# Kernel tuning notes

Hardware: AMD Instinct MI355X
Metric: run time of the kernel (lower is better)

Reference implementation:

```python
import jax, jax.numpy as jnp
import numpy as np

B, N, L, D = 4, 2048, 12, 128  # batch, nodes, in_len, d_model


def _glorot(key, shape):
    fan_in = shape[0]
    return jax.random.normal(key, shape, dtype=jnp.float32) / jnp.sqrt(jnp.float32(fan_in))


def setup_inputs() -> dict:
    key = jax.random.key(0)
    ks = jax.random.split(key, 12)
    x = jax.random.normal(ks[0], (B, N, L, D), dtype=jnp.float32)
    adj = jax.random.uniform(ks[1], (N, N), dtype=jnp.float32)  # dense weighted adjacency
    # mlp2: Linear(L*D -> D)
    W_mlp2 = _glorot(ks[2], (L * D, D)); b_mlp2 = jnp.zeros((D,), jnp.float32)
    # GNN: three DenseSAGEConv layers (lin_rel on aggregated, lin_root on self)
    Wr1 = _glorot(ks[3], (D, D)); Wo1 = _glorot(ks[4], (D, D)); b1 = jnp.zeros((D,), jnp.float32)
    Wr2 = _glorot(ks[5], (D, D)); Wo2 = _glorot(ks[6], (D, D)); b2 = jnp.zeros((D,), jnp.float32)
    Wr3 = _glorot(ks[7], (D, D)); Wo3 = _glorot(ks[8], (D, D)); b3 = jnp.zeros((D,), jnp.float32)
    # mlp1: Linear(D -> L*D)
    W_mlp1 = _glorot(ks[9], (D, L * D)); b_mlp1 = jnp.zeros((L * D,), jnp.float32)
    return {"x": x, "adj": adj, "W_mlp2": W_mlp2, "b_mlp2": b_mlp2,
            "Wr1": Wr1, "Wo1": Wo1, "b1": b1,
            "Wr2": Wr2, "Wo2": Wo2, "b2": b2,
            "Wr3": Wr3, "Wo3": Wo3, "b3": b3,
            "W_mlp1": W_mlp1, "b_mlp1": b_mlp1}


def reference(x, adj, W_mlp2, b_mlp2, Wr1, Wo1, b1, Wr2, Wo2, b2, Wr3, Wo3, b3, W_mlp1, b_mlp1):
    b_, n_, l_, d_ = x.shape
    xf = x.reshape(b_, n_, l_ * d_)                      # 'b n l d -> b n (l d)'
    h = xf @ W_mlp2 + b_mlp2                             # mlp2: (B,N,D)
    deg = jnp.clip(adj.sum(axis=-1, keepdims=True), 1.0, None)  # (N,1)

    def sage(hin, Wr, Wo, bb):
        # mean neighbor aggregation: (adj @ h) / deg, then rel + root linear
        agg = jnp.einsum('mn,bnd->bmd', adj, hin) / deg
        return agg @ Wr + hin @ Wo + bb

    h = jax.nn.relu(sage(h, Wr1, Wo1, b1))
    h = jax.nn.relu(sage(h, Wr2, Wo2, b2))
    h = sage(h, Wr3, Wo3, b3)                            # gnn1_embed output (B,N,D)
    out = h @ W_mlp1 + b_mlp1                            # mlp1: (B,N,L*D)
    return out
```

## Files before the change

### kernel.cpp

```cpp
#include <hip/hip_runtime.h>

typedef __attribute__((ext_vector_type(8))) short short8;
typedef __attribute__((ext_vector_type(4))) short short4v;
typedef __attribute__((ext_vector_type(4))) float floatx4;

__device__ inline short to_bf16s(float f) {
    unsigned u = __builtin_bit_cast(unsigned, f);
    unsigned r = u + 0x7FFFu + ((u >> 16) & 1u);
    return (short)(r >> 16);
}

__device__ inline void dma16(const short* g, short* l) {
    __builtin_amdgcn_global_load_lds(
        (const __attribute__((address_space(1))) unsigned int*)(const void*)g,
        (__attribute__((address_space(3))) unsigned int*)(void*)l,
        16, 0, 0);
}

template <typename T> struct Ld8;
template <> struct Ld8<short> {
    static __device__ inline short8 load(const short* p) { return *(const short8*)p; }
};
template <> struct Ld8<float> {
    static __device__ inline short8 load(const float* p) {
        float4 f0 = *(const float4*)p;
        float4 f1 = *(const float4*)(p + 4);
        short8 r;
        r[0] = to_bf16s(f0.x); r[1] = to_bf16s(f0.y);
        r[2] = to_bf16s(f0.z); r[3] = to_bf16s(f0.w);
        r[4] = to_bf16s(f1.x); r[5] = to_bf16s(f1.y);
        r[6] = to_bf16s(f1.z); r[7] = to_bf16s(f1.w);
        return r;
    }
};

struct PrepArgs {
    const float* adj;
    const float* W2; const float* W1;
    const float* Wr0; const float* Wo0;
    const float* Wr1; const float* Wo1;
    const float* Wr2; const float* Wo2;
    short* adjS; short* W2T; short* W1T;
    short* BigB0; short* BigB1; short* BigB2;
};

__global__ __launch_bounds__(256) void prep(PrepArgs p) {
    int bid = blockIdx.x;
    if (bid < 2048) {
        const float* src = p.adj + (size_t)bid * 2048;
        float s = 0.f;
        for (int c = threadIdx.x; c < 2048; c += 256) s += src[c];
        __shared__ float red[256];
        red[threadIdx.x] = s;
        __syncthreads();
        for (int st = 128; st > 0; st >>= 1) {
            if (threadIdx.x < st) red[threadIdx.x] += red[threadIdx.x + st];
            __syncthreads();
        }
        float d = red[0];
        d = d < 1.f ? 1.f : d;
        float inv = 1.f / d;
        short* dst = p.adjS + (size_t)bid * 2048;
        for (int c = threadIdx.x; c < 2048; c += 256) dst[c] = to_bf16s(src[c] * inv);
        return;
    }
    int t = bid - 2048;
    __shared__ short tile[32][33];
    int tx = threadIdx.x & 31, ty0 = threadIdx.x >> 5;
    const float* in; int C_; int bx, by;
    short* outp; int outld, copies, copystride, outofs;
    if (t < 192) {
        bx = (t & 3) * 32; by = (t >> 2) * 32; in = p.W2; C_ = 128;
        outp = p.W2T; outld = 1536; copies = 1; copystride = 0; outofs = 0;
    } else if (t < 384) {
        int u = t - 192; bx = (u % 48) * 32; by = (u / 48) * 32; in = p.W1; C_ = 1536;
        outp = p.W1T; outld = 128; copies = 1; copystride = 0; outofs = 0;
    } else {
        int u = t - 384; int l = u / 32; int v = u % 32;
        const float* Wr[3] = {p.Wr0, p.Wr1, p.Wr2};
        const float* Wo[3] = {p.Wo0, p.Wo1, p.Wo2};
        short* BB[3] = {p.BigB0, p.BigB1, p.BigB2};
        outp = BB[l]; outld = 640; C_ = 128;
        if (v < 16) { in = Wr[l]; bx = (v & 3) * 32; by = (v >> 2) * 32;
                      copies = 4; copystride = 128; outofs = 0; }
        else { v -= 16; in = Wo[l]; bx = (v & 3) * 32; by = (v >> 2) * 32;
               copies = 1; copystride = 0; outofs = 512; }
    }
    for (int i = ty0; i < 32; i += 8)
        tile[i][tx] = to_bf16s(in[(size_t)(by + i) * C_ + bx + tx]);
    __syncthreads();
    for (int i = ty0; i < 32; i += 8) {
        short v = tile[tx][i];
        for (int c = 0; c < copies; ++c)
            outp[(size_t)(bx + i) * outld + (by + tx) + outofs + c * copystride] = v;
    }
}

#define LDSTR 72

template <typename TA, int RELU, int ROWMAP, int HTW>
__global__ __launch_bounds__(256) void gemmT(
    const TA* __restrict__ A, int lda,
    const short* __restrict__ B, int ldb, int kTiles,
    const float* __restrict__ bias,
    short* __restrict__ C, int ldc, int colofs,
    short* __restrict__ HT) {
    __shared__ __align__(16) short lds[2 * 96 * LDSTR];

    int tid = threadIdx.x;
    int blockM = blockIdx.x * 32;
    int blockN = blockIdx.y * 64;

    int srow = tid >> 3;
    int scol = (tid & 7) * 8;

    const TA* Abase = A + (size_t)blockM * lda;
    const short* Bbase = B + (size_t)blockN * ldb;

    short8 ra, rb0, rb1;
    ra  = Ld8<TA>::load(Abase + (size_t)srow * lda + scol);
    rb0 = Ld8<short>::load(Bbase + (size_t)srow * ldb + scol);
    rb1 = Ld8<short>::load(Bbase + (size_t)(srow + 32) * ldb + scol);

    floatx4 acc[2];
    #pragma unroll
    for (int j = 0; j < 2; ++j)
        #pragma unroll
        for (int r = 0; r < 4; ++r) acc[j][r] = 0.f;

    int lane = tid & 63;
    int w = tid >> 6;
    int wr = w >> 1, wc = w & 1;
    int quad = lane >> 4, l15 = lane & 15;

    for (int it = 0; it < kTiles; ++it) {
        short* As = lds + (it & 1) * (96 * LDSTR);
        short* Bs = As + 32 * LDSTR;
        *(short8*)(As + srow * LDSTR + scol) = ra;
        *(short8*)(Bs + srow * LDSTR + scol) = rb0;
        *(short8*)(Bs + (srow + 32) * LDSTR + scol) = rb1;
        __syncthreads();
        if (it + 1 < kTiles) {
            int ko = (it + 1) * 64;
            ra  = Ld8<TA>::load(Abase + (size_t)srow * lda + ko + scol);
            rb0 = Ld8<short>::load(Bbase + (size_t)srow * ldb + ko + scol);
            rb1 = Ld8<short>::load(Bbase + (size_t)(srow + 32) * ldb + ko + scol);
        }
        const short* Arow = As + (wr * 16 + l15) * LDSTR;
        const short* Brow = Bs + (wc * 32 + l15) * LDSTR;
        #pragma unroll
        for (int ks = 0; ks < 2; ++ks) {
            int kof = ks * 32 + quad * 8;
            short8 a0 = *(const short8*)(Arow + kof);
            short8 b0 = *(const short8*)(Brow + kof);
            short8 b1 = *(const short8*)(Brow + 16 * LDSTR + kof);
            acc[0] = __builtin_amdgcn_mfma_f32_16x16x32_bf16(a0, b0, acc[0], 0, 0, 0);
            acc[1] = __builtin_amdgcn_mfma_f32_16x16x32_bf16(a0, b1, acc[1], 0, 0, 0);
        }
        __syncthreads();
    }

    #pragma unroll
    for (int tj = 0; tj < 2; ++tj) {
        int col = blockN + wc * 32 + tj * 16 + l15;
        float bv = bias[col];
        int m0 = blockM + wr * 16 + quad * 4;
        short4v pk;
        #pragma unroll
        for (int r = 0; r < 4; ++r) {
            int m = m0 + r;
            float xv = acc[tj][r] + bv;
            if (RELU) xv = xv > 0.f ? xv : 0.f;
            short v = to_bf16s(xv);
            pk[r] = v;
            int orow = ROWMAP ? (((m & 2047) << 2) | (m >> 11)) : m;
            C[(size_t)orow * ldc + col + colofs] = v;
            if (HTW && !ROWMAP) {
                HT[(size_t)((m & 3) * 128 + col) * 2048 + (m >> 2)] = v;
            }
        }
        if (HTW && ROWMAP) {
            int b = m0 >> 11, n0 = m0 & 2047;
            *(short4v*)(HT + (size_t)(b * 128 + col) * 2048 + n0) = pk;
        }
    }
}

__global__ __launch_bounds__(256) void gemmS(const short* __restrict__ A,
                                             const short* __restrict__ B,
                                             short* __restrict__ C) {
    __shared__ __align__(16) short As[64 * 64];
    __shared__ __align__(16) short Bs[128 * 64];

    int tid = threadIdx.x;
    int blockM = blockIdx.x * 64;
    int blockN = blockIdx.y * 128;
    int kz = blockIdx.z * 512;

    const short* Ab = A + (size_t)(blockM + (tid >> 3)) * 2048 + kz + (tid & 7) * 8;
    const short* Bb = B + (size_t)(blockN + (tid >> 3)) * 2048 + kz + (tid & 7) * 8;
    short* Al = As + tid * 8;
    short* Bl = Bs + tid * 8;

    floatx4 acc[2][4];
    #pragma unroll
    for (int i = 0; i < 2; ++i)
        #pragma unroll
        for (int j = 0; j < 4; ++j)
            #pragma unroll
            for (int r = 0; r < 4; ++r) acc[i][j][r] = 0.f;

    int lane = tid & 63;
    int w = tid >> 6;
    int wr = w >> 1, wc = w & 1;
    int quad = lane >> 4, l15 = lane & 15;

    for (int it = 0; it < 8; ++it) {
        const short* Ag = Ab + it * 64;
        const short* Bg = Bb + it * 64;
        dma16(Ag, Al);
        dma16(Ag + (size_t)32 * 2048, Al + 2048);
        #pragma unroll
        for (int r = 0; r < 4; ++r)
            dma16(Bg + (size_t)r * 32 * 2048, Bl + r * 2048);
        __syncthreads();
        const short* Ar = As + (wr * 32 + l15) * 64;
        const short* Br = Bs + (wc * 64 + l15) * 64;
        #pragma unroll
        for (int ks = 0; ks < 2; ++ks) {
            int kof = ks * 32 + quad * 8;
            short8 af[2], bfr[4];
            #pragma unroll
            for (int i = 0; i < 2; ++i) af[i] = *(const short8*)(Ar + i * 16 * 64 + kof);
            #pragma unroll
            for (int j = 0; j < 4; ++j) bfr[j] = *(const short8*)(Br + j * 16 * 64 + kof);
            #pragma unroll
            for (int i = 0; i < 2; ++i)
                #pragma unroll
                for (int j = 0; j < 4; ++j)
                    acc[i][j] = __builtin_amdgcn_mfma_f32_16x16x32_bf16(af[i], bfr[j], acc[i][j], 0, 0, 0);
        }
        __syncthreads();
    }

    int colofs = blockIdx.z * 128;
    #pragma unroll
    for (int ti = 0; ti < 2; ++ti) {
        #pragma unroll
        for (int tj = 0; tj < 4; ++tj) {
            int j = blockN + wc * 64 + tj * 16 + l15;
            int jhi = j >> 7, jlo = j & 127;
            int row0 = blockM + wr * 32 + ti * 16 + quad * 4;
            #pragma unroll
            for (int r = 0; r < 4; ++r) {
                int m = row0 + r;
                C[(size_t)(m * 4 + jhi) * 640 + jlo + colofs] = to_bf16s(acc[ti][tj][r]);
            }
        }
    }
}

template <int MODE>
__global__ __launch_bounds__(256) void gemm128(
    const short* __restrict__ A, int lda,
    const short* __restrict__ B, int ldb,
    int kChunkIters, const float* __restrict__ bias,
    void* __restrict__ Cv, int ldc) {
    __shared__ __align__(16) short As[128 * 64];
    __shared__ __align__(16) short Bs[128 * 64];

    int tid = threadIdx.x;
    int blockM = blockIdx.x * 128;
    int blockN = blockIdx.y * 128;
    int kz = blockIdx.z * kChunkIters * 64;

    const short* Ab = A + (size_t)(blockM + (tid >> 3)) * lda + kz + (tid & 7) * 8;
    const short* Bb = B + (size_t)(blockN + (tid >> 3)) * ldb + kz + (tid & 7) * 8;
    short* Al = As + tid * 8;
    short* Bl = Bs + tid * 8;

    floatx4 acc[4][4];
    #pragma unroll
    for (int i = 0; i < 4; ++i)
        #pragma unroll
        for (int j = 0; j < 4; ++j)
            #pragma unroll
            for (int r = 0; r < 4; ++r) acc[i][j][r] = 0.f;

    int lane = tid & 63;
    int w = tid >> 6;
    int wr = w >> 1, wc = w & 1;
    int quad = lane >> 4, l15 = lane & 15;

    for (int it = 0; it < kChunkIters; ++it) {
        const short* Ag = Ab + it * 64;
        const short* Bg = Bb + it * 64;
        #pragma unroll
        for (int r = 0; r < 4; ++r) {
            dma16(Ag + (size_t)r * 32 * lda, Al + r * 2048);
            dma16(Bg + (size_t)r * 32 * ldb, Bl + r * 2048);
        }
        __syncthreads();
        const short* Ar = As + (wr * 64 + l15) * 64;
        const short* Br = Bs + (wc * 64 + l15) * 64;
        #pragma unroll
        for (int ks = 0; ks < 2; ++ks) {
            int kof = ks * 32 + quad * 8;
            short8 af[4], bfr[4];
            #pragma unroll
            for (int i = 0; i < 4; ++i) af[i] = *(const short8*)(Ar + i * 16 * 64 + kof);
            #pragma unroll
            for (int j = 0; j < 4; ++j) bfr[j] = *(const short8*)(Br + j * 16 * 64 + kof);
            #pragma unroll
            for (int i = 0; i < 4; ++i)
                #pragma unroll
                for (int j = 0; j < 4; ++j)
                    acc[i][j] = __builtin_amdgcn_mfma_f32_16x16x32_bf16(af[i], bfr[j], acc[i][j], 0, 0, 0);
        }
        __syncthreads();
    }

    {
        float* Cf = (float*)Cv;
        #pragma unroll
        for (int ti = 0; ti < 4; ++ti) {
            #pragma unroll
            for (int tj = 0; tj < 4; ++tj) {
                int col = blockN + wc * 64 + tj * 16 + l15;
                float bv = bias[col];
                int row0 = blockM + wr * 64 + ti * 16 + quad * 4;
                #pragma unroll
                for (int r = 0; r < 4; ++r) {
                    int mp = row0 + r;
                    int orow = ((mp & 3) << 11) | (mp >> 2);
                    Cf[(size_t)orow * ldc + col] = acc[ti][tj][r] + bv;
                }
            }
        }
    }
}

extern "C" void kernel_launch(void* const* d_in, const int* in_sizes, int n_in,
                              void* d_out, int out_size, void* d_ws, size_t ws_size,
                              hipStream_t stream) {
    const float* x      = (const float*)d_in[0];
    const float* adj    = (const float*)d_in[1];
    const float* W_mlp2 = (const float*)d_in[2];
    const float* b_mlp2 = (const float*)d_in[3];
    const float* Wr1    = (const float*)d_in[4];
    const float* Wo1    = (const float*)d_in[5];
    const float* b1     = (const float*)d_in[6];
    const float* Wr2    = (const float*)d_in[7];
    const float* Wo2    = (const float*)d_in[8];
    const float* b2     = (const float*)d_in[9];
    const float* Wr3    = (const float*)d_in[10];
    const float* Wo3    = (const float*)d_in[11];
    const float* b3     = (const float*)d_in[12];
    const float* W_mlp1 = (const float*)d_in[13];
    const float* b_mlp1 = (const float*)d_in[14];
    float* out = (float*)d_out;

    char* ws = (char*)d_ws;
    size_t off = 0;
    auto alloc = [&](size_t bytes) -> char* {
        char* p = ws + off;
        off = (off + bytes + 255) & ~(size_t)255;
        return p;
    };
    short* W2T  = (short*)alloc(128 * 1536 * 2);
    short* W1T  = (short*)alloc(1536 * 128 * 2);
    short* BigB[3];
    for (int l = 0; l < 3; ++l) BigB[l] = (short*)alloc(128 * 640 * 2);
    short* adjS = (short*)alloc((size_t)2048 * 2048 * 2);
    short* big[4];
    for (int l = 0; l < 4; ++l) big[l] = (short*)alloc((size_t)8192 * 640 * 2);
    short* HT = (short*)alloc((size_t)512 * 2048 * 2);

    dim3 blk(256);

    PrepArgs pa{adj, W_mlp2, W_mlp1, Wr1, Wo1, Wr2, Wo2, Wr3, Wo3,
                adjS, W2T, W1T, BigB[0], BigB[1], BigB[2]};
    prep<<<2528, blk, 0, stream>>>(pa);

    gemmT<float, 0, 1, 1><<<dim3(256, 2), blk, 0, stream>>>(
        x, 1536, W2T, 1536, 24, b_mlp2, big[0], 640, 512, HT);

    for (int l = 0; l < 3; ++l) {
        gemmS<<<dim3(32, 4, 4), blk, 0, stream>>>(adjS, HT, big[l]);
        if (l == 0)
            gemmT<short, 1, 0, 1><<<dim3(256, 2), blk, 0, stream>>>(
                big[0], 640, BigB[0], 640, 10, b1, big[1], 640, 512, HT);
        else if (l == 1)
            gemmT<short, 1, 0, 1><<<dim3(256, 2), blk, 0, stream>>>(
                big[1], 640, BigB[1], 640, 10, b2, big[2], 640, 512, HT);
        else
            gemmT<short, 0, 0, 0><<<dim3(256, 2), blk, 0, stream>>>(
                big[2], 640, BigB[2], 640, 10, b3, big[3], 640, 512, nullptr);
    }

    gemm128<2><<<dim3(64, 12, 1), blk, 0, stream>>>(
        big[3] + 512, 640, W1T, 128, 2, b_mlp1, out, 1536);
}
```

Before: 225.6 us.

## Load MFMA fragments directly from global memory, dropping LDS staging in all GEMMs

The three GEMM kernels (gemmT, gemmS, and the final gemm128, now gemmL) no longer stage tiles through shared memory with barriers and direct-to-LDS DMA. Each lane now loads its bf16 fragments straight from global memory in fully unrolled K loops with compile-time trip counts. This removes LDS traffic and __syncthreads stalls, and relies on L1/L2 caching to supply the data reuse that the shared tiles used to provide. The risk is more redundant global or cache traffic, uncoalesced 16-byte per-lane accesses, and higher register pressure from the full unrolling.

```diff
diff --git a/kernel.cpp b/kernel.cpp
--- a/kernel.cpp
+++ b/kernel.cpp
@@ -8,13 +8,6 @@
     unsigned u = __builtin_bit_cast(unsigned, f);
     unsigned r = u + 0x7FFFu + ((u >> 16) & 1u);
     return (short)(r >> 16);
-}
-
-__device__ inline void dma16(const short* g, short* l) {
-    __builtin_amdgcn_global_load_lds(
-        (const __attribute__((address_space(1))) unsigned int*)(const void*)g,
-        (__attribute__((address_space(3))) unsigned int*)(void*)l,
-        16, 0, 0);
 }
 
 template <typename T> struct Ld8;
@@ -96,68 +89,40 @@
     }
 }
 
-#define LDSTR 72
-
-template <typename TA, int RELU, int ROWMAP, int HTW>
+template <typename TA, int KS, int RELU, int ROWMAP, int HTW>
 __global__ __launch_bounds__(256) void gemmT(
     const TA* __restrict__ A, int lda,
-    const short* __restrict__ B, int ldb, int kTiles,
+    const short* __restrict__ B, int ldb,
     const float* __restrict__ bias,
     short* __restrict__ C, int ldc, int colofs,
     short* __restrict__ HT) {
-    __shared__ __align__(16) short lds[2 * 96 * LDSTR];
-
     int tid = threadIdx.x;
-    int blockM = blockIdx.x * 32;
-    int blockN = blockIdx.y * 64;
-
-    int srow = tid >> 3;
-    int scol = (tid & 7) * 8;
-
-    const TA* Abase = A + (size_t)blockM * lda;
-    const short* Bbase = B + (size_t)blockN * ldb;
-
-    short8 ra, rb0, rb1;
-    ra  = Ld8<TA>::load(Abase + (size_t)srow * lda + scol);
-    rb0 = Ld8<short>::load(Bbase + (size_t)srow * ldb + scol);
-    rb1 = Ld8<short>::load(Bbase + (size_t)(srow + 32) * ldb + scol);
-
-    floatx4 acc[2];
-    #pragma unroll
-    for (int j = 0; j < 2; ++j)
-        #pragma unroll
-        for (int r = 0; r < 4; ++r) acc[j][r] = 0.f;
-
     int lane = tid & 63;
     int w = tid >> 6;
     int wr = w >> 1, wc = w & 1;
     int quad = lane >> 4, l15 = lane & 15;
 
-    for (int it = 0; it < kTiles; ++it) {
-        short* As = lds + (it & 1) * (96 * LDSTR);
-        short* Bs = As + 32 * LDSTR;
-        *(short8*)(As + srow * LDSTR + scol) = ra;
-        *(short8*)(Bs + srow * LDSTR + scol) = rb0;
-        *(short8*)(Bs + (srow + 32) * LDSTR + scol) = rb1;
-        __syncthreads();
-        if (it + 1 < kTiles) {
-            int ko = (it + 1) * 64;
-            ra  = Ld8<TA>::load(Abase + (size_t)srow * lda + ko + scol);
-            rb0 = Ld8<short>::load(Bbase + (size_t)srow * ldb + ko + scol);
-            rb1 = Ld8<short>::load(Bbase + (size_t)(srow + 32) * ldb + ko + scol);
-        }
-        const short* Arow = As + (wr * 16 + l15) * LDSTR;
-        const short* Brow = Bs + (wc * 32 + l15) * LDSTR;
-        #pragma unroll
-        for (int ks = 0; ks < 2; ++ks) {
-            int kof = ks * 32 + quad * 8;
-            short8 a0 = *(const short8*)(Arow + kof);
-            short8 b0 = *(const short8*)(Brow + kof);
-            short8 b1 = *(const short8*)(Brow + 16 * LDSTR + kof);
-            acc[0] = __builtin_amdgcn_mfma_f32_16x16x32_bf16(a0, b0, acc[0], 0, 0, 0);
-            acc[1] = __builtin_amdgcn_mfma_f32_16x16x32_bf16(a0, b1, acc[1], 0, 0, 0);
-        }
-        __syncthreads();
+    int blockM = blockIdx.x * 32;
+    int blockN = blockIdx.y * 64;
+
+    const TA* Ap = A + (size_t)(blockM + wr * 16 + l15) * lda + quad * 8;
+    const short* Bp0 = B + (size_t)(blockN + wc * 32 + l15) * ldb + quad * 8;
+    const short* Bp1 = Bp0 + (size_t)16 * ldb;
+
+    floatx4 acc[2];
+    #pragma unroll
+    for (int j = 0; j < 2; ++j)
+        #pragma unroll
+        for (int r = 0; r < 4; ++r) acc[j][r] = 0.f;
+
+    #pragma unroll
+    for (int t = 0; t < KS; ++t) {
+        int kof = t * 32;
+        short8 a0 = Ld8<TA>::load(Ap + kof);
+        short8 b0 = *(const short8*)(Bp0 + kof);
+        short8 b1 = *(const short8*)(Bp1 + kof);
+        acc[0] = __builtin_amdgcn_mfma_f32_16x16x32_bf16(a0, b0, acc[0], 0, 0, 0);
+        acc[1] = __builtin_amdgcn_mfma_f32_16x16x32_bf16(a0, b1, acc[1], 0, 0, 0);
     }
 
     #pragma unroll
@@ -189,58 +154,45 @@
 __global__ __launch_bounds__(256) void gemmS(const short* __restrict__ A,
                                              const short* __restrict__ B,
                                              short* __restrict__ C) {
-    __shared__ __align__(16) short As[64 * 64];
-    __shared__ __align__(16) short Bs[128 * 64];
-
     int tid = threadIdx.x;
-    int blockM = blockIdx.x * 64;
-    int blockN = blockIdx.y * 128;
-    int kz = blockIdx.z * 512;
-
-    const short* Ab = A + (size_t)(blockM + (tid >> 3)) * 2048 + kz + (tid & 7) * 8;
-    const short* Bb = B + (size_t)(blockN + (tid >> 3)) * 2048 + kz + (tid & 7) * 8;
-    short* Al = As + tid * 8;
-    short* Bl = Bs + tid * 8;
-
-    floatx4 acc[2][4];
-    #pragma unroll
-    for (int i = 0; i < 2; ++i)
-        #pragma unroll
-        for (int j = 0; j < 4; ++j)
-            #pragma unroll
-            for (int r = 0; r < 4; ++r) acc[i][j][r] = 0.f;
-
     int lane = tid & 63;
     int w = tid >> 6;
     int wr = w >> 1, wc = w & 1;
     int quad = lane >> 4, l15 = lane & 15;
-
-    for (int it = 0; it < 8; ++it) {
-        const short* Ag = Ab + it * 64;
-        const short* Bg = Bb + it * 64;
-        dma16(Ag, Al);
-        dma16(Ag + (size_t)32 * 2048, Al + 2048);
-        #pragma unroll
-        for (int r = 0; r < 4; ++r)
-            dma16(Bg + (size_t)r * 32 * 2048, Bl + r * 2048);
-        __syncthreads();
-        const short* Ar = As + (wr * 32 + l15) * 64;
-        const short* Br = Bs + (wc * 64 + l15) * 64;
-        #pragma unroll
-        for (int ks = 0; ks < 2; ++ks) {
-            int kof = ks * 32 + quad * 8;
-            short8 af[2], bfr[4];
-            #pragma unroll
-            for (int i = 0; i < 2; ++i) af[i] = *(const short8*)(Ar + i * 16 * 64 + kof);
-            #pragma unroll
-            for (int j = 0; j < 4; ++j) bfr[j] = *(const short8*)(Br + j * 16 * 64 + kof);
-            #pragma unroll
-            for (int i = 0; i < 2; ++i)
-                #pragma unroll
-                for (int j = 0; j < 4; ++j)
-                    acc[i][j] = __builtin_amdgcn_mfma_f32_16x16x32_bf16(af[i], bfr[j], acc[i][j], 0, 0, 0);
-        }
-        __syncthreads();
+    int kz = blockIdx.z * 512;
+
+    const short* Ap0 = A + (size_t)(blockIdx.x * 64 + wr * 32 + l15) * 2048 + kz + quad * 8;
+    const short* Ap1 = Ap0 + (size_t)16 * 2048;
+    const short* Bp0 = B + (size_t)(blockIdx.y * 128 + wc * 64 + l15) * 2048 + kz + quad * 8;
+    const short* Bp1 = Bp0 + (size_t)16 * 2048;
+    const short* Bp2 = Bp0 + (size_t)32 * 2048;
+    const short* Bp3 = Bp0 + (size_t)48 * 2048;
+
+    floatx4 acc[2][4];
+    #pragma unroll
+    for (int i = 0; i < 2; ++i)
+        #pragma unroll
+        for (int j = 0; j < 4; ++j)
+            #pragma unroll
+            for (int r = 0; r < 4; ++r) acc[i][j][r] = 0.f;
+
+    #pragma unroll
+    for (int t = 0; t < 16; ++t) {
+        int kof = t * 32;
+        short8 a0 = *(const short8*)(Ap0 + kof);
+        short8 a1 = *(const short8*)(Ap1 + kof);
+        short8 b0 = *(const short8*)(Bp0 + kof);
+        short8 b1 = *(const short8*)(Bp1 + kof);
+        short8 b2 = *(const short8*)(Bp2 + kof);
+        short8 b3 = *(const short8*)(Bp3 + kof);
+        acc[0][0] = __builtin_amdgcn_mfma_f32_16x16x32_bf16(a0, b0, acc[0][0], 0, 0, 0);
+        acc[0][1] = __builtin_amdgcn_mfma_f32_16x16x32_bf16(a0, b1, acc[0][1], 0, 0, 0);
+        acc[0][2] = __builtin_amdgcn_mfma_f32_16x16x32_bf16(a0, b2, acc[0][2], 0, 0, 0);
+        acc[0][3] = __builtin_amdgcn_mfma_f32_16x16x32_bf16(a0, b3, acc[0][3], 0, 0, 0);
+        acc[1][0] = __builtin_amdgcn_mfma_f32_16x16x32_bf16(a1, b0, acc[1][0], 0, 0, 0);
+        acc[1][1] = __builtin_amdgcn_mfma_f32_16x16x32_bf16(a1, b1, acc[1][1], 0, 0, 0);
+        acc[1][2] = __builtin_amdgcn_mfma_f32_16x16x32_bf16(a1, b2, acc[1][2], 0, 0, 0);
+        acc[1][3] = __builtin_amdgcn_mfma_f32_16x16x32_bf16(a1, b3, acc[1][3], 0, 0, 0);
     }
 
     int colofs = blockIdx.z * 128;
@@ -248,9 +200,9 @@
     for (int ti = 0; ti < 2; ++ti) {
         #pragma unroll
         for (int tj = 0; tj < 4; ++tj) {
-            int j = blockN + wc * 64 + tj * 16 + l15;
+            int j = blockIdx.y * 128 + wc * 64 + tj * 16 + l15;
             int jhi = j >> 7, jlo = j & 127;
-            int row0 = blockM + wr * 32 + ti * 16 + quad * 4;
+            int row0 = blockIdx.x * 64 + wr * 32 + ti * 16 + quad * 4;
             #pragma unroll
             for (int r = 0; r < 4; ++r) {
                 int m = row0 + r;
@@ -260,81 +212,63 @@
     }
 }
 
-template <int MODE>
-__global__ __launch_bounds__(256) void gemm128(
-    const short* __restrict__ A, int lda,
-    const short* __restrict__ B, int ldb,
-    int kChunkIters, const float* __restrict__ bias,
-    void* __restrict__ Cv, int ldc) {
-    __shared__ __align__(16) short As[128 * 64];
-    __shared__ __align__(16) short Bs[128 * 64];
-
+__global__ __launch_bounds__(256) void gemmL(const short* __restrict__ A,
+                                             const short* __restrict__ B,
+                                             const float* __restrict__ bias,
+                                             float* __restrict__ C) {
     int tid = threadIdx.x;
-    int blockM = blockIdx.x * 128;
-    int blockN = blockIdx.y * 128;
-    int kz = blockIdx.z * kChunkIters * 64;
-
-    const short* Ab = A + (size_t)(blockM + (tid >> 3)) * lda + kz + (tid & 7) * 8;
-    const short* Bb = B + (size_t)(blockN + (tid >> 3)) * ldb + kz + (tid & 7) * 8;
-    short* Al = As + tid * 8;
-    short* Bl = Bs + tid * 8;
-
-    floatx4 acc[4][4];
-    #pragma unroll
-    for (int i = 0; i < 4; ++i)
-        #pragma unroll
-        for (int j = 0; j < 4; ++j)
-            #pragma unroll
-            for (int r = 0; r < 4; ++r) acc[i][j][r] = 0.f;
-
     int lane = tid & 63;
     int w = tid >> 6;
     int wr = w >> 1, wc = w & 1;
     int quad = lane >> 4, l15 = lane & 15;
 
-    for (int it = 0; it < kChunkIters; ++it) {
-        const short* Ag = Ab + it * 64;
-        const short* Bg = Bb + it * 64;
-        #pragma unroll
-        for (int r = 0; r < 4; ++r) {
-            dma16(Ag + (size_t)r * 32 * lda, Al + r * 2048);
-            dma16(Bg + (size_t)r * 32 * ldb, Bl + r * 2048);
-        }
-        __syncthreads();
-        const short* Ar = As + (wr * 64 + l15) * 64;
-        const short* Br = Bs + (wc * 64 + l15) * 64;
-        #pragma unroll
-        for (int ks = 0; ks < 2; ++ks) {
-            int kof = ks * 32 + quad * 8;
-            short8 af[4], bfr[4];
-            #pragma unroll
-            for (int i = 0; i < 4; ++i) af[i] = *(const short8*)(Ar + i * 16 * 64 + kof);
-            #pragma unroll
-            for (int j = 0; j < 4; ++j) bfr[j] = *(const short8*)(Br + j * 16 * 64 + kof);
-            #pragma unroll
-            for (int i = 0; i < 4; ++i)
-                #pragma unroll
-                for (int j = 0; j < 4; ++j)
-                    acc[i][j] = __builtin_amdgcn_mfma_f32_16x16x32_bf16(af[i], bfr[j], acc[i][j], 0, 0, 0);
-        }
-        __syncthreads();
-    }
-
-    {
-        float* Cf = (float*)Cv;
-        #pragma unroll
-        for (int ti = 0; ti < 4; ++ti) {
-            #pragma unroll
-            for (int tj = 0; tj < 4; ++tj) {
-                int col = blockN + wc * 64 + tj * 16 + l15;
-                float bv = bias[col];
-                int row0 = blockM + wr * 64 + ti * 16 + quad * 4;
-                #pragma unroll
-                for (int r = 0; r < 4; ++r) {
-                    int mp = row0 + r;
-                    int orow = ((mp & 3) << 11) | (mp >> 2);
-                    Cf[(size_t)orow * ldc + col] = acc[ti][tj][r] + bv;
-                }
+    int blockM = blockIdx.x * 128;
+    int blockN = blockIdx.y * 128;
+
+    const short* Ap[4];
+    const short* Bp[4];
+    #pragma unroll
+    for (int i = 0; i < 4; ++i)
+        Ap[i] = A + (size_t)(blockM + wr * 64 + i * 16 + l15) * 640 + quad * 8;
+    #pragma unroll
+    for (int j = 0; j < 4; ++j)
+        Bp[j] = B + (size_t)(blockN + wc * 64 + j * 16 + l15) * 128 + quad * 8;
+
+    floatx4 acc[4][4];
+    #pragma unroll
+    for (int i = 0; i < 4; ++i)
+        #pragma unroll
+        for (int j = 0; j < 4; ++j)
+            #pragma unroll
+            for (int r = 0; r < 4; ++r) acc[i][j][r] = 0.f;
+
+    #pragma unroll
+    for (int t = 0; t < 4; ++t) {
+        int kof = t * 32;
+        short8 af[4], bf[4];
+        #pragma unroll
+        for (int i = 0; i < 4; ++i) af[i] = *(const short8*)(Ap[i] + kof);
+        #pragma unroll
+        for (int j = 0; j < 4; ++j) bf[j] = *(const short8*)(Bp[j] + kof);
+        #pragma unroll
+        for (int i = 0; i < 4; ++i)
+            #pragma unroll
+            for (int j = 0; j < 4; ++j)
+                acc[i][j] = __builtin_amdgcn_mfma_f32_16x16x32_bf16(af[i], bf[j], acc[i][j], 0, 0, 0);
+    }
+
+    #pragma unroll
+    for (int ti = 0; ti < 4; ++ti) {
+        #pragma unroll
+        for (int tj = 0; tj < 4; ++tj) {
+            int col = blockN + wc * 64 + tj * 16 + l15;
+            float bv = bias[col];
+            int row0 = blockM + wr * 64 + ti * 16 + quad * 4;
+            #pragma unroll
+            for (int r = 0; r < 4; ++r) {
+                int mp = row0 + r;
+                int orow = ((mp & 3) << 11) | (mp >> 2);
+                C[(size_t)orow * 1536 + col] = acc[ti][tj][r] + bv;
             }
         }
     }
@@ -382,22 +316,21 @@
                 adjS, W2T, W1T, BigB[0], BigB[1], BigB[2]};
     prep<<<2528, blk, 0, stream>>>(pa);
 
-    gemmT<float, 0, 1, 1><<<dim3(256, 2), blk, 0, stream>>>(
-        x, 1536, W2T, 1536, 24, b_mlp2, big[0], 640, 512, HT);
+    gemmT<float, 48, 0, 1, 1><<<dim3(256, 2), blk, 0, stream>>>(
+        x, 1536, W2T, 1536, b_mlp2, big[0], 640, 512, HT);
 
     for (int l = 0; l < 3; ++l) {
         gemmS<<<dim3(32, 4, 4), blk, 0, stream>>>(adjS, HT, big[l]);
         if (l == 0)
-            gemmT<short, 1, 0, 1><<<dim3(256, 2), blk, 0, stream>>>(
-                big[0], 640, BigB[0], 640, 10, b1, big[1], 640, 512, HT);
+            gemmT<short, 20, 1, 0, 1><<<dim3(256, 2), blk, 0, stream>>>(
+                big[0], 640, BigB[0], 640, b1, big[1], 640, 512, HT);
         else if (l == 1)
-            gemmT<short, 1, 0, 1><<<dim3(256, 2), blk, 0, stream>>>(
-                big[1], 640, BigB[1], 640, 10, b2, big[2], 640, 512, HT);
+            gemmT<short, 20, 1, 0, 1><<<dim3(256, 2), blk, 0, stream>>>(
+                big[1], 640, BigB[1], 640, b2, big[2], 640, 512, HT);
         else
-            gemmT<short, 0, 0, 0><<<dim3(256, 2), blk, 0, stream>>>(
-                big[2], 640, BigB[2], 640, 10, b3, big[3], 640, 512, nullptr);
-    }
-
-    gemm128<2><<<dim3(64, 12, 1), blk, 0, stream>>>(
-        big[3] + 512, 640, W1T, 128, 2, b_mlp1, out, 1536);
-}
+            gemmT<short, 20, 0, 0, 0><<<dim3(256, 2), blk, 0, stream>>>(
+                big[2], 640, BigB[2], 640, b3, big[3], 640, 512, nullptr);
+    }
+
+    gemmL<<<dim3(64, 12), blk, 0, stream>>>(big[3] + 512, W1T, b_mlp1, out);
+}
```

Result: slower. 317.4 us (+40.7%).

## Double-buffer adjacency GEMM LDS and load full K in final projection

Applied to the files above, without the earlier changes.

The adjacency aggregation GEMM now uses two LDS buffers, so the DMA for the next K tile is issued while MFMAs run on the current one. The final mlp1 projection becomes a dedicated kernel that loads the whole K=128 slice into LDS at once, with one barrier and no K loop. The trailing barrier in the gemmT loop is also removed to cut synchronisation. Double buffering doubles gemmS LDS use, which can lower occupancy. Dropping the gemmT barrier may let fast warps overwrite LDS that slower warps are still reading.

```diff
diff --git a/kernel.cpp b/kernel.cpp
--- a/kernel.cpp
+++ b/kernel.cpp
@@ -157,7 +157,6 @@
             acc[0] = __builtin_amdgcn_mfma_f32_16x16x32_bf16(a0, b0, acc[0], 0, 0, 0);
             acc[1] = __builtin_amdgcn_mfma_f32_16x16x32_bf16(a0, b1, acc[1], 0, 0, 0);
         }
-        __syncthreads();
     }
 
     #pragma unroll
@@ -189,18 +188,14 @@
 __global__ __launch_bounds__(256) void gemmS(const short* __restrict__ A,
                                              const short* __restrict__ B,
                                              short* __restrict__ C) {
-    __shared__ __align__(16) short As[64 * 64];
-    __shared__ __align__(16) short Bs[128 * 64];
+    __shared__ __align__(16) short As[2][64 * 64];
+    __shared__ __align__(16) short Bs[2][128 * 64];
 
     int tid = threadIdx.x;
-    int blockM = blockIdx.x * 64;
-    int blockN = blockIdx.y * 128;
     int kz = blockIdx.z * 512;
 
-    const short* Ab = A + (size_t)(blockM + (tid >> 3)) * 2048 + kz + (tid & 7) * 8;
-    const short* Bb = B + (size_t)(blockN + (tid >> 3)) * 2048 + kz + (tid & 7) * 8;
-    short* Al = As + tid * 8;
-    short* Bl = Bs + tid * 8;
+    const short* Ab = A + (size_t)(blockIdx.x * 64 + (tid >> 3)) * 2048 + kz + (tid & 7) * 8;
+    const short* Bb = B + (size_t)(blockIdx.y * 128 + (tid >> 3)) * 2048 + kz + (tid & 7) * 8;
 
     floatx4 acc[2][4];
     #pragma unroll
@@ -215,17 +210,24 @@
     int wr = w >> 1, wc = w & 1;
     int quad = lane >> 4, l15 = lane & 15;
 
-    for (int it = 0; it < 8; ++it) {
+    auto stage = [&](int p, int it) {
         const short* Ag = Ab + it * 64;
         const short* Bg = Bb + it * 64;
-        dma16(Ag, Al);
-        dma16(Ag + (size_t)32 * 2048, Al + 2048);
+        dma16(Ag, &As[p][tid * 8]);
+        dma16(Ag + (size_t)32 * 2048, &As[p][tid * 8 + 2048]);
         #pragma unroll
         for (int r = 0; r < 4; ++r)
-            dma16(Bg + (size_t)r * 32 * 2048, Bl + r * 2048);
-        __syncthreads();
-        const short* Ar = As + (wr * 32 + l15) * 64;
-        const short* Br = Bs + (wc * 64 + l15) * 64;
+            dma16(Bg + (size_t)r * 32 * 2048, &Bs[p][tid * 8 + r * 2048]);
+    };
+
+    stage(0, 0);
+    __syncthreads();
+
+    for (int it = 0; it < 8; ++it) {
+        int p = it & 1;
+        if (it + 1 < 8) stage(p ^ 1, it + 1);
+        const short* Ar = &As[p][(wr * 32 + l15) * 64];
+        const short* Br = &Bs[p][(wc * 64 + l15) * 64];
         #pragma unroll
         for (int ks = 0; ks < 2; ++ks) {
             int kof = ks * 32 + quad * 8;
@@ -248,9 +250,9 @@
     for (int ti = 0; ti < 2; ++ti) {
         #pragma unroll
         for (int tj = 0; tj < 4; ++tj) {
-            int j = blockN + wc * 64 + tj * 16 + l15;
+            int j = blockIdx.y * 128 + wc * 64 + tj * 16 + l15;
             int jhi = j >> 7, jlo = j & 127;
-            int row0 = blockM + wr * 32 + ti * 16 + quad * 4;
+            int row0 = blockIdx.x * 64 + wr * 32 + ti * 16 + quad * 4;
             #pragma unroll
             for (int r = 0; r < 4; ++r) {
                 int m = row0 + r;
@@ -260,24 +262,24 @@
     }
 }
 
-template <int MODE>
-__global__ __launch_bounds__(256) void gemm128(
-    const short* __restrict__ A, int lda,
-    const short* __restrict__ B, int ldb,
-    int kChunkIters, const float* __restrict__ bias,
-    void* __restrict__ Cv, int ldc) {
-    __shared__ __align__(16) short As[128 * 64];
-    __shared__ __align__(16) short Bs[128 * 64];
+__global__ __launch_bounds__(256) void gemmL(const short* __restrict__ A,
+                                             const short* __restrict__ B,
+                                             const float* __restrict__ bias,
+                                             float* __restrict__ C) {
+    __shared__ __align__(16) short As[128 * 128];
+    __shared__ __align__(16) short Bs[128 * 128];
 
     int tid = threadIdx.x;
     int blockM = blockIdx.x * 128;
     int blockN = blockIdx.y * 128;
-    int kz = blockIdx.z * kChunkIters * 64;
-
-    const short* Ab = A + (size_t)(blockM + (tid >> 3)) * lda + kz + (tid & 7) * 8;
-    const short* Bb = B + (size_t)(blockN + (tid >> 3)) * ldb + kz + (tid & 7) * 8;
-    short* Al = As + tid * 8;
-    short* Bl = Bs + tid * 8;
+
+    const short* Ag = A + (size_t)(blockM + (tid >> 4)) * 640 + (tid & 15) * 8;
+    const short* Bg = B + (size_t)(blockN + (tid >> 4)) * 128 + (tid & 15) * 8;
+    #pragma unroll
+    for (int r = 0; r < 8; ++r) {
+        dma16(Ag + (size_t)r * 16 * 640, &As[tid * 8 + r * 2048]);
+        dma16(Bg + (size_t)r * 16 * 128, &Bs[tid * 8 + r * 2048]);
+    }
 
     floatx4 acc[4][4];
     #pragma unroll
@@ -292,49 +294,37 @@
     int wr = w >> 1, wc = w & 1;
     int quad = lane >> 4, l15 = lane & 15;
 
-    for (int it = 0; it < kChunkIters; ++it) {
-        const short* Ag = Ab + it * 64;
-        const short* Bg = Bb + it * 64;
-        #pragma unroll
-        for (int r = 0; r < 4; ++r) {
-            dma16(Ag + (size_t)r * 32 * lda, Al + r * 2048);
-            dma16(Bg + (size_t)r * 32 * ldb, Bl + r * 2048);
-        }
-        __syncthreads();
-        const short* Ar = As + (wr * 64 + l15) * 64;
-        const short* Br = Bs + (wc * 64 + l15) * 64;
-        #pragma unroll
-        for (int ks = 0; ks < 2; ++ks) {
-            int kof = ks * 32 + quad * 8;
-            short8 af[4], bfr[4];
-            #pragma unroll
-            for (int i = 0; i < 4; ++i) af[i] = *(const short8*)(Ar + i * 16 * 64 + kof);
-            #pragma unroll
-            for (int j = 0; j < 4; ++j) bfr[j] = *(const short8*)(Br + j * 16 * 64 + kof);
-            #pragma unroll
-            for (int i = 0; i < 4; ++i)
-                #pragma unroll
-                for (int j = 0; j < 4; ++j)
-                    acc[i][j] = __builtin_amdgcn_mfma_f32_16x16x32_bf16(af[i], bfr[j], acc[i][j], 0, 0, 0);
-        }
-        __syncthreads();
-    }
-
-    {
-        float* Cf = (float*)Cv;
-        #pragma unroll
-        for (int ti = 0; ti < 4; ++ti) {
-            #pragma unroll
-            for (int tj = 0; tj < 4; ++tj) {
-                int col = blockN + wc * 64 + tj * 16 + l15;
-                float bv = bias[col];
-                int row0 = blockM + wr * 64 + ti * 16 + quad * 4;
-                #pragma unroll
-                for (int r = 0; r < 4; ++r) {
-                    int mp = row0 + r;
-                    int orow = ((mp & 3) << 11) | (mp >> 2);
-                    Cf[(size_t)orow * ldc + col] = acc[ti][tj][r] + bv;
-                }
+    __syncthreads();
+
+    const short* Ar = As + (wr * 64 + l15) * 128;
+    const short* Br = Bs + (wc * 64 + l15) * 128;
+    #pragma unroll
+    for (int t = 0; t < 4; ++t) {
+        int kof = t * 32 + quad * 8;
+        short8 af[4], bf[4];
+        #pragma unroll
+        for (int i = 0; i < 4; ++i) af[i] = *(const short8*)(Ar + i * 16 * 128 + kof);
+        #pragma unroll
+        for (int j = 0; j < 4; ++j) bf[j] = *(const short8*)(Br + j * 16 * 128 + kof);
+        #pragma unroll
+        for (int i = 0; i < 4; ++i)
+            #pragma unroll
+            for (int j = 0; j < 4; ++j)
+                acc[i][j] = __builtin_amdgcn_mfma_f32_16x16x32_bf16(af[i], bf[j], acc[i][j], 0, 0, 0);
+    }
+
+    #pragma unroll
+    for (int ti = 0; ti < 4; ++ti) {
+        #pragma unroll
+        for (int tj = 0; tj < 4; ++tj) {
+            int col = blockN + wc * 64 + tj * 16 + l15;
+            float bv = bias[col];
+            int row0 = blockM + wr * 64 + ti * 16 + quad * 4;
+            #pragma unroll
+            for (int r = 0; r < 4; ++r) {
+                int mp = row0 + r;
+                int orow = ((mp & 3) << 11) | (mp >> 2);
+                C[(size_t)orow * 1536 + col] = acc[ti][tj][r] + bv;
             }
         }
     }
@@ -398,6 +388,5 @@
                 big[2], 640, BigB[2], 640, 10, b3, big[3], 640, 512, nullptr);
     }
 
-    gemm128<2><<<dim3(64, 12, 1), blk, 0, stream>>>(
-        big[3] + 512, 640, W1T, 128, 2, b_mlp1, out, 1536);
-}
+    gemmL<<<dim3(64, 12), blk, 0, stream>>>(big[3] + 512, W1T, b_mlp1, out);
+}
```

New measurement: 230.8 us. 2.3% more time.

## Add triple-buffered async LDS pipeline to gemmS and unroll gemmT by two tiles

Applied to the files above, without the earlier changes.

gemmS now keeps three LDS slots and issues the DMA loads two tiles ahead. A vmcnt wait replaces the full syncthreads, so global loads overlap with MFMA work. gemmT is unrolled by two with register prefetch two tiles deep into alternating buffers, and drops one barrier per tile. gemm128 is renamed and simplified to gemmL with no functional change. The extra LDS in gemmS (about 72KB) may reduce occupancy, and gemmT's unroll assumes kTiles is even (24 and 10 both are).

```diff
diff --git a/kernel.cpp b/kernel.cpp
--- a/kernel.cpp
+++ b/kernel.cpp
@@ -117,10 +117,12 @@
     const TA* Abase = A + (size_t)blockM * lda;
     const short* Bbase = B + (size_t)blockN * ldb;
 
-    short8 ra, rb0, rb1;
-    ra  = Ld8<TA>::load(Abase + (size_t)srow * lda + scol);
-    rb0 = Ld8<short>::load(Bbase + (size_t)srow * ldb + scol);
-    rb1 = Ld8<short>::load(Bbase + (size_t)(srow + 32) * ldb + scol);
+    short8 a0_  = Ld8<TA>::load(Abase + (size_t)srow * lda + scol);
+    short8 b00_ = Ld8<short>::load(Bbase + (size_t)srow * ldb + scol);
+    short8 b10_ = Ld8<short>::load(Bbase + (size_t)(srow + 32) * ldb + scol);
+    short8 a1_  = Ld8<TA>::load(Abase + (size_t)srow * lda + 64 + scol);
+    short8 b01_ = Ld8<short>::load(Bbase + (size_t)srow * ldb + 64 + scol);
+    short8 b11_ = Ld8<short>::load(Bbase + (size_t)(srow + 32) * ldb + 64 + scol);
 
     floatx4 acc[2];
     #pragma unroll
@@ -133,31 +135,58 @@
     int wr = w >> 1, wc = w & 1;
     int quad = lane >> 4, l15 = lane & 15;
 
-    for (int it = 0; it < kTiles; ++it) {
-        short* As = lds + (it & 1) * (96 * LDSTR);
-        short* Bs = As + 32 * LDSTR;
-        *(short8*)(As + srow * LDSTR + scol) = ra;
-        *(short8*)(Bs + srow * LDSTR + scol) = rb0;
-        *(short8*)(Bs + (srow + 32) * LDSTR + scol) = rb1;
-        __syncthreads();
-        if (it + 1 < kTiles) {
-            int ko = (it + 1) * 64;
-            ra  = Ld8<TA>::load(Abase + (size_t)srow * lda + ko + scol);
-            rb0 = Ld8<short>::load(Bbase + (size_t)srow * ldb + ko + scol);
-            rb1 = Ld8<short>::load(Bbase + (size_t)(srow + 32) * ldb + ko + scol);
-        }
-        const short* Arow = As + (wr * 16 + l15) * LDSTR;
-        const short* Brow = Bs + (wc * 32 + l15) * LDSTR;
-        #pragma unroll
-        for (int ks = 0; ks < 2; ++ks) {
-            int kof = ks * 32 + quad * 8;
-            short8 a0 = *(const short8*)(Arow + kof);
-            short8 b0 = *(const short8*)(Brow + kof);
-            short8 b1 = *(const short8*)(Brow + 16 * LDSTR + kof);
-            acc[0] = __builtin_amdgcn_mfma_f32_16x16x32_bf16(a0, b0, acc[0], 0, 0, 0);
-            acc[1] = __builtin_amdgcn_mfma_f32_16x16x32_bf16(a0, b1, acc[1], 0, 0, 0);
-        }
-        __syncthreads();
+    short* buf0 = lds;
+    short* buf1 = lds + 96 * LDSTR;
+
+    for (int it = 0; it < kTiles; it += 2) {
+        *(short8*)(buf0 + srow * LDSTR + scol) = a0_;
+        *(short8*)(buf0 + (32 + srow) * LDSTR + scol) = b00_;
+        *(short8*)(buf0 + (64 + srow) * LDSTR + scol) = b10_;
+        asm volatile("s_waitcnt lgkmcnt(0)" ::: "memory");
+        __builtin_amdgcn_s_barrier();
+        if (it + 2 < kTiles) {
+            int ko = (it + 2) * 64;
+            a0_  = Ld8<TA>::load(Abase + (size_t)srow * lda + ko + scol);
+            b00_ = Ld8<short>::load(Bbase + (size_t)srow * ldb + ko + scol);
+            b10_ = Ld8<short>::load(Bbase + (size_t)(srow + 32) * ldb + ko + scol);
+        }
+        {
+            const short* Arow = buf0 + (wr * 16 + l15) * LDSTR;
+            const short* Brow = buf0 + (32 + wc * 32 + l15) * LDSTR;
+            #pragma unroll
+            for (int ks = 0; ks < 2; ++ks) {
+                int kof = ks * 32 + quad * 8;
+                short8 a0 = *(const short8*)(Arow + kof);
+                short8 b0 = *(const short8*)(Brow + kof);
+                short8 b1 = *(const short8*)(Brow + 16 * LDSTR + kof);
+                acc[0] = __builtin_amdgcn_mfma_f32_16x16x32_bf16(a0, b0, acc[0], 0, 0, 0);
+                acc[1] = __builtin_amdgcn_mfma_f32_16x16x32_bf16(a0, b1, acc[1], 0, 0, 0);
+            }
+        }
+        *(short8*)(buf1 + srow * LDSTR + scol) = a1_;
+        *(short8*)(buf1 + (32 + srow) * LDSTR + scol) = b01_;
+        *(short8*)(buf1 + (64 + srow) * LDSTR + scol) = b11_;
+        asm volatile("s_waitcnt lgkmcnt(0)" ::: "memory");
+        __builtin_amdgcn_s_barrier();
+        if (it + 3 < kTiles) {
+            int ko = (it + 3) * 64;
+            a1_  = Ld8<TA>::load(Abase + (size_t)srow * lda + ko + scol);
+            b01_ = Ld8<short>::load(Bbase + (size_t)srow * ldb + ko + scol);
+            b11_ = Ld8<short>::load(Bbase + (size_t)(srow + 32) * ldb + ko + scol);
+        }
+        {
+            const short* Arow = buf1 + (wr * 16 + l15) * LDSTR;
+            const short* Brow = buf1 + (32 + wc * 32 + l15) * LDSTR;
+            #pragma unroll
+            for (int ks = 0; ks < 2; ++ks) {
+                int kof = ks * 32 + quad * 8;
+                short8 a0 = *(const short8*)(Arow + kof);
+                short8 b0 = *(const short8*)(Brow + kof);
+                short8 b1 = *(const short8*)(Brow + 16 * LDSTR + kof);
+                acc[0] = __builtin_amdgcn_mfma_f32_16x16x32_bf16(a0, b0, acc[0], 0, 0, 0);
+                acc[1] = __builtin_amdgcn_mfma_f32_16x16x32_bf16(a0, b1, acc[1], 0, 0, 0);
+            }
+        }
     }
 
     #pragma unroll
@@ -189,18 +218,13 @@
 __global__ __launch_bounds__(256) void gemmS(const short* __restrict__ A,
                                              const short* __restrict__ B,
                                              short* __restrict__ C) {
-    __shared__ __align__(16) short As[64 * 64];
-    __shared__ __align__(16) short Bs[128 * 64];
+    __shared__ __align__(16) short lds3[3 * 12288];
 
     int tid = threadIdx.x;
-    int blockM = blockIdx.x * 64;
-    int blockN = blockIdx.y * 128;
     int kz = blockIdx.z * 512;
 
-    const short* Ab = A + (size_t)(blockM + (tid >> 3)) * 2048 + kz + (tid & 7) * 8;
-    const short* Bb = B + (size_t)(blockN + (tid >> 3)) * 2048 + kz + (tid & 7) * 8;
-    short* Al = As + tid * 8;
-    short* Bl = Bs + tid * 8;
+    const short* Ab = A + (size_t)(blockIdx.x * 64 + (tid >> 3)) * 2048 + kz + (tid & 7) * 8;
+    const short* Bb = B + (size_t)(blockIdx.y * 128 + (tid >> 3)) * 2048 + kz + (tid & 7) * 8;
 
     floatx4 acc[2][4];
     #pragma unroll
@@ -215,17 +239,33 @@
     int wr = w >> 1, wc = w & 1;
     int quad = lane >> 4, l15 = lane & 15;
 
-    for (int it = 0; it < 8; ++it) {
+    auto stage = [&](int slot, int it) {
+        short* As = lds3 + slot * 12288;
+        short* Bs = As + 4096;
         const short* Ag = Ab + it * 64;
         const short* Bg = Bb + it * 64;
-        dma16(Ag, Al);
-        dma16(Ag + (size_t)32 * 2048, Al + 2048);
+        dma16(Ag, As + tid * 8);
+        dma16(Ag + (size_t)32 * 2048, As + tid * 8 + 2048);
         #pragma unroll
         for (int r = 0; r < 4; ++r)
-            dma16(Bg + (size_t)r * 32 * 2048, Bl + r * 2048);
-        __syncthreads();
+            dma16(Bg + (size_t)r * 32 * 2048, Bs + tid * 8 + r * 2048);
+    };
+
+    stage(0, 0);
+    stage(1, 1);
+
+    int slot = 0;
+    for (int it = 0; it < 8; ++it) {
+        if (it < 7) asm volatile("s_waitcnt vmcnt(6)" ::: "memory");
+        else        asm volatile("s_waitcnt vmcnt(0)" ::: "memory");
+        __builtin_amdgcn_s_barrier();
+        if (it + 2 < 8) {
+            int s2 = slot + 2; if (s2 >= 3) s2 -= 3;
+            stage(s2, it + 2);
+        }
+        const short* As = lds3 + slot * 12288;
         const short* Ar = As + (wr * 32 + l15) * 64;
-        const short* Br = Bs + (wc * 64 + l15) * 64;
+        const short* Br = As + 4096 + (wc * 64 + l15) * 64;
         #pragma unroll
         for (int ks = 0; ks < 2; ++ks) {
             int kof = ks * 32 + quad * 8;
@@ -240,7 +280,7 @@
                 for (int j = 0; j < 4; ++j)
                     acc[i][j] = __builtin_amdgcn_mfma_f32_16x16x32_bf16(af[i], bfr[j], acc[i][j], 0, 0, 0);
         }
-        __syncthreads();
+        slot = (slot + 1 == 3) ? 0 : slot + 1;
     }
 
     int colofs = blockIdx.z * 128;
@@ -248,9 +288,9 @@
     for (int ti = 0; ti < 2; ++ti) {
         #pragma unroll
         for (int tj = 0; tj < 4; ++tj) {
-            int j = blockN + wc * 64 + tj * 16 + l15;
+            int j = blockIdx.y * 128 + wc * 64 + tj * 16 + l15;
             int jhi = j >> 7, jlo = j & 127;
-            int row0 = blockM + wr * 32 + ti * 16 + quad * 4;
+            int row0 = blockIdx.x * 64 + wr * 32 + ti * 16 + quad * 4;
             #pragma unroll
             for (int r = 0; r < 4; ++r) {
                 int m = row0 + r;
@@ -260,22 +300,20 @@
     }
 }
 
-template <int MODE>
-__global__ __launch_bounds__(256) void gemm128(
+__global__ __launch_bounds__(256) void gemmL(
     const short* __restrict__ A, int lda,
     const short* __restrict__ B, int ldb,
     int kChunkIters, const float* __restrict__ bias,
-    void* __restrict__ Cv, int ldc) {
+    float* __restrict__ Cf, int ldc) {
     __shared__ __align__(16) short As[128 * 64];
     __shared__ __align__(16) short Bs[128 * 64];
 
     int tid = threadIdx.x;
     int blockM = blockIdx.x * 128;
     int blockN = blockIdx.y * 128;
-    int kz = blockIdx.z * kChunkIters * 64;
-
-    const short* Ab = A + (size_t)(blockM + (tid >> 3)) * lda + kz + (tid & 7) * 8;
-    const short* Bb = B + (size_t)(blockN + (tid >> 3)) * ldb + kz + (tid & 7) * 8;
+
+    const short* Ab = A + (size_t)(blockM + (tid >> 3)) * lda + (tid & 7) * 8;
+    const short* Bb = B + (size_t)(blockN + (tid >> 3)) * ldb + (tid & 7) * 8;
     short* Al = As + tid * 8;
     short* Bl = Bs + tid * 8;
 
@@ -320,21 +358,18 @@
         __syncthreads();
     }
 
-    {
-        float* Cf = (float*)Cv;
-        #pragma unroll
-        for (int ti = 0; ti < 4; ++ti) {
-            #pragma unroll
-            for (int tj = 0; tj < 4; ++tj) {
-                int col = blockN + wc * 64 + tj * 16 + l15;
-                float bv = bias[col];
-                int row0 = blockM + wr * 64 + ti * 16 + quad * 4;
-                #pragma unroll
-                for (int r = 0; r < 4; ++r) {
-                    int mp = row0 + r;
-                    int orow = ((mp & 3) << 11) | (mp >> 2);
-                    Cf[(size_t)orow * ldc + col] = acc[ti][tj][r] + bv;
-                }
+    #pragma unroll
+    for (int ti = 0; ti < 4; ++ti) {
+        #pragma unroll
+        for (int tj = 0; tj < 4; ++tj) {
+            int col = blockN + wc * 64 + tj * 16 + l15;
+            float bv = bias[col];
+            int row0 = blockM + wr * 64 + ti * 16 + quad * 4;
+            #pragma unroll
+            for (int r = 0; r < 4; ++r) {
+                int mp = row0 + r;
+                int orow = ((mp & 3) << 11) | (mp >> 2);
+                Cf[(size_t)orow * ldc + col] = acc[ti][tj][r] + bv;
             }
         }
     }
@@ -398,6 +433,5 @@
                 big[2], 640, BigB[2], 640, 10, b3, big[3], 640, 512, nullptr);
     }
 
-    gemm128<2><<<dim3(64, 12, 1), blk, 0, stream>>>(
-        big[3] + 512, 640, W1T, 128, 2, b_mlp1, out, 1536);
-}
+    gemmL<<<dim3(64, 12), blk, 0, stream>>>(big[3] + 512, 640, W1T, 128, 2, b_mlp1, out, 1536);
+}
```

Measured after the change: 219.9 us. -2.5%, faster.
